# Optimization experiments

Measured on AMD Instinct MI355X. Metric: run time of the kernel, lower is better.

## Reference

```python
import jax, jax.numpy as jnp
import numpy as np

K = 7      # number of neighbor volumes (init k)
PS = 7     # patch size (unfold.ps / wpsum.ps)
WS = 13    # search window side -> O = WS*WS candidates per query
WR = WS // 2
EPS = 1e-6


def setup_inputs() -> dict:
    key = jax.random.key(0)
    k1, k2, k3, k4 = jax.random.split(key, 4)
    C, E, H, W = 64, 32, 128, 128
    return {
        "x": jax.random.normal(k1, (C, H, W), jnp.float32),
        "xe": jax.random.normal(k2, (E, H, W), jnp.float32),
        "ye": jax.random.normal(k3, (E, H, W), jnp.float32),
        "log_temp": 0.1 * jax.random.normal(k4, (1, H, W), jnp.float32),
    }


def _box_sum(img, ps):
    # img: [B, H, W] -> centered ps x ps box sum with zero padding, same shape
    kern = jnp.ones((1, 1, ps, ps), img.dtype)
    return jax.lax.conv_general_dilated(img[:, None], kern, (1, 1), "SAME")[:, 0]


def _forward(x, xe, ye, log_temp):
    C, H, W_ = x.shape
    E = xe.shape[0]
    offs = np.stack(np.meshgrid(np.arange(WS), np.arange(WS), indexing="ij"), -1).reshape(-1, 2)
    O = offs.shape[0]
    dis = jnp.asarray(offs[:, 0]); djs = jnp.asarray(offs[:, 1])

    xe_pad = jnp.pad(xe, ((0, 0), (WR, WR), (WR, WR)))
    x_pad = jnp.pad(x, ((0, 0), (WR, WR), (WR, WR)))

    # ---- search: per-candidate patch SSD between query/database embeddings ----
    def per_off_dist(di, dj):
        xs = jax.lax.dynamic_slice(xe_pad, (0, di, dj), (E, H, W_))
        return jnp.sum((ye - xs) ** 2, axis=0)  # [H, W] pixel-wise sq dist

    diff2 = jax.vmap(per_off_dist)(dis, djs)        # [O, H, W]
    dists = -_box_sum(diff2, PS)                    # patch SSD, negated

    # ---- temperature: avgpool of log_temp over the ps x ps patch (avgpool=True) ----
    lt = _box_sum(log_temp, PS) / float(PS * PS)    # [1, H, W]
    temp = jnp.exp(lt)                              # temp_bias=1 -> log bias 0

    # ---- NeuralNearestNeighbors: k rounds of temp-softmax with exclusion ----
    logits = dists / temp                           # [O, H, W]
    Ws = []
    for _ in range(K):  # small structural loop over k neighbor volumes
        w = jax.nn.softmax(logits, axis=0)
        Ws.append(w)
        logits = logits + jnp.log(jnp.clip(1.0 - w, EPS))
    Wk = jnp.stack(Ws, 0)                           # [K, O, H, W]

    # ---- wpsum + fold fused: for stride-1 centered patches the patch offset
    # cancels, so out[k,c,y] = sum_o boxsum_ps(W[k,o])[y] * x[c, y + off(o)] ----
    Wsum = _box_sum(Wk.reshape(K * O, H, W_), PS).reshape(K, O, H, W_)
    Wsum_o = jnp.moveaxis(Wsum, 1, 0)               # [O, K, H, W]

    def body(out, inp):
        di, dj, wso = inp
        xs = jax.lax.dynamic_slice(x_pad, (0, di, dj), (C, H, W_))
        return out + wso[:, None] * xs[None], None  # [K, C, H, W]

    out0 = jnp.zeros((K, C, H, W_), x.dtype)
    out, _ = jax.lax.scan(body, out0, (dis, djs, Wsum_o))
    return out.reshape(K * C, H, W_)


def reference(x, xe, ye, log_temp):
    return _forward(x, xe, ye, log_temp)
```

## Files before the change

### kernel.cpp

```cpp
#include <hip/hip_runtime.h>
#include <hip/hip_bf16.h>
#include <hip/hip_fp16.h>

#define HW 16384

using u16 = unsigned short;
using u32 = unsigned int;
typedef __attribute__((ext_vector_type(2))) float f32x2;

__device__ __forceinline__ u16 f2h(float f) {
    __half h = __float2half(f);
    return __builtin_bit_cast(u16, h);
}
__device__ __forceinline__ void dot2acc(float& acc, u32 a, u32 b) {
    asm("v_dot2_f32_f16 %0, %1, %2, %0" : "+v"(acc) : "v"(a), "v"(b));
}
#define SELLO 0x05040100u
#define SELHI 0x07060302u

__global__ __launch_bounds__(256) void k_prep(
        const float* __restrict__ x, const float* __restrict__ xe,
        const float* __restrict__ ye,
        u16* __restrict__ xh, float* __restrict__ xeT,
        float* __restrict__ yeT, float* __restrict__ nx, float* __restrict__ ny) {
    int y = blockIdx.x * 256 + threadIdx.x;

#pragma unroll
    for (int c = 0; c < 64; c++)
        xh[c * HW + y] = f2h(x[c * HW + y]);

    float sx = 0.f, sy = 0.f;
#pragma unroll
    for (int e0 = 0; e0 < 32; e0 += 4) {
        float4 v = make_float4(xe[(e0 + 0) * HW + y], xe[(e0 + 1) * HW + y],
                               xe[(e0 + 2) * HW + y], xe[(e0 + 3) * HW + y]);
        *reinterpret_cast<float4*>(xeT + y * 32 + e0) = v;
        sx += v.x * v.x + v.y * v.y + v.z * v.z + v.w * v.w;
        float4 u = make_float4(ye[(e0 + 0) * HW + y], ye[(e0 + 1) * HW + y],
                               ye[(e0 + 2) * HW + y], ye[(e0 + 3) * HW + y]);
        *reinterpret_cast<float4*>(yeT + y * 32 + e0) = u;
        sy += u.x * u.x + u.y * u.y + u.z * u.z + u.w * u.w;
    }
    nx[y] = sx;
    ny[y] = sy;
}

__global__ __launch_bounds__(256) void k_norms(
        const float* __restrict__ ny, const float* __restrict__ lt,
        float2* __restrict__ st) {
    int y = blockIdx.x * 256 + threadIdx.x;
    int py = y >> 7, px = y & 127;
    float s = 0.f, t = 0.f;
    for (int dy = -3; dy <= 3; dy++)
        for (int dx = -3; dx <= 3; dx++) {
            int yy = py + dy, xx = px + dx;
            if ((unsigned)yy < 128u && (unsigned)xx < 128u) {
                int p = yy * 128 + xx;
                s += ny[p];
                t += lt[p];
            }
        }
    float tinv = __expf(-t * (1.0f / 49.0f));
    st[y] = make_float2(tinv, tinv * s);
}

__global__ __launch_bounds__(1024) void k_logits(
        const float* __restrict__ xeT, const float* __restrict__ yeT,
        const float* __restrict__ nxg, const float2* __restrict__ st,
        float* __restrict__ logits) {
#pragma clang fp contract(fast)
    __shared__ __align__(16) char arena[123904];
    float* s_xe = (float*)arena;
    float* s_nx = (float*)(arena + 95744);
    float* s_d2 = (float*)(arena + 98736);
    float* s_hs = (float*)arena;

    int di = blockIdx.x;
    int tile = blockIdx.y;
    int h0 = (tile >> 3) * 16, w0 = (tile & 7) * 16;
    int gr0 = h0 + di - 9, gc0 = w0 - 9;
    int tid = threadIdx.x;

    for (int idx = tid; idx < 748 * 8; idx += 1024) {
        int cell = idx >> 3, q = idx & 7;
        int r = cell / 34, c = cell - r * 34;
        int gy = gr0 + r, gx = gc0 + c;
        float4 v = make_float4(0.f, 0.f, 0.f, 0.f);
        if ((unsigned)gy < 128u && (unsigned)gx < 128u)
            v = *reinterpret_cast<const float4*>(xeT + (size_t)(gy * 128 + gx) * 32 + q * 4);
        *reinterpret_cast<float4*>(s_xe + cell * 32 + ((q ^ (cell & 7)) << 2)) = v;
    }
    for (int idx = tid; idx < 748; idx += 1024) {
        int r = idx / 34, c = idx - r * 34;
        int gy = gr0 + r, gx = gc0 + c;
        float v = 0.f;
        if ((unsigned)gy < 128u && (unsigned)gx < 128u) v = nxg[gy * 128 + gx];
        s_nx[idx] = v;
    }
    __syncthreads();

    if (tid < 484) {
        int zr = tid / 22, zc = tid - zr * 22;
        int gy = h0 - 3 + zr, gx = w0 - 3 + zc;
        bool zin = ((unsigned)gy < 128u) && ((unsigned)gx < 128u);
        f32x2 yv[16];
#pragma unroll
        for (int j = 0; j < 16; j++) yv[j] = (f32x2){0.f, 0.f};
        if (zin) {
            const float* yp = yeT + (size_t)(gy * 128 + gx) * 32;
#pragma unroll
            for (int j = 0; j < 8; j++) {
                float4 t = *reinterpret_cast<const float4*>(yp + j * 4);
                yv[2 * j] = (f32x2){t.x, t.y};
                yv[2 * j + 1] = (f32x2){t.z, t.w};
            }
        }
        int cell0 = zr * 34 + zc;
#pragma unroll
        for (int dj = 0; dj < 13; dj++) {
            int cell = cell0 + dj;
            const float* bp = s_xe + cell * 32;
            int sw = cell & 7;
            f32x2 a0 = {0.f, 0.f}, a1 = {0.f, 0.f};
#pragma unroll
            for (int q = 0; q < 8; q++) {
                float4 xv = *reinterpret_cast<const float4*>(bp + ((q ^ sw) << 2));
                a0 += ((f32x2){xv.x, xv.y}) * yv[2 * q];
                a1 += ((f32x2){xv.z, xv.w}) * yv[2 * q + 1];
            }
            float cr = a0.x + a0.y + a1.x + a1.y;
            float d2v = fmaf(-2.f, cr, s_nx[cell]);
            s_d2[dj * 484 + tid] = zin ? d2v : 0.f;
        }
    }
    __syncthreads();

    for (int idx = tid; idx < 4576; idx += 1024) {
        int dj = idx / 352, rem = idx - dj * 352;
        int r = rem >> 4, c = rem & 15;
        const float* p = s_d2 + dj * 484 + r * 22 + c;
        float s = p[0] + p[1] + p[2] + p[3] + p[4] + p[5] + p[6];
        s_hs[(dj * 22 + r) * 16 + c] = s;
    }
    __syncthreads();

    for (int idx = tid; idx < 3328; idx += 1024) {
        int dj = idx >> 8, rem = idx & 255;
        int i = rem >> 4, jj = rem & 15;
        const float* p = s_hs + (dj * 22 + i) * 16 + jj;
        float s = p[0] + p[16] + p[32] + p[48] + p[64] + p[80] + p[96];
        int y = (h0 + i) * 128 + (w0 + jj);
        float2 ab = st[y];
        logits[(di * 13 + dj) * HW + y] = -fmaf(ab.x, s, ab.y);
    }
}

__global__ __launch_bounds__(256) void k_softmax(
        const float* __restrict__ logits, u16* __restrict__ Wkt) {
    __shared__ float s_lg[169 * 34];
    int tid = threadIdx.x;
    int y0 = blockIdx.x * 32;
    for (int idx = tid; idx < 169 * 32; idx += 256) {
        int o = idx >> 5, p = idx & 31;
        s_lg[o * 34 + p] = logits[o * HW + y0 + p];
    }
    __syncthreads();
    int pix = tid >> 3, t = tid & 7;
    int y = y0 + pix;
    float l[22];
#pragma unroll
    for (int j = 0; j < 22; j++) {
        int o = t + 8 * j;
        l[j] = (o < 169) ? s_lg[o * 34 + pix] : -3e38f;
    }
    u32 wp0[22], wp1[22], wp2[22], wp3[22];
#pragma unroll
    for (int j = 0; j < 22; j++) { wp0[j] = 0u; wp1[j] = 0u; wp2[j] = 0u; wp3[j] = 0u; }

    float e[22];
#pragma unroll
    for (int k = 0; k < 7; k++) {
        float m = -3e38f;
#pragma unroll
        for (int j = 0; j < 22; j++) m = fmaxf(m, l[j]);
        m = fmaxf(m, __shfl_xor(m, 1));
        m = fmaxf(m, __shfl_xor(m, 2));
        m = fmaxf(m, __shfl_xor(m, 4));
        float s = 0.f;
#pragma unroll
        for (int j = 0; j < 22; j++) { e[j] = __expf(l[j] - m); s += e[j]; }
        s += __shfl_xor(s, 1);
        s += __shfl_xor(s, 2);
        s += __shfl_xor(s, 4);
        float rs = 1.0f / s;
#pragma unroll
        for (int j = 0; j < 22; j++) {
            float w = e[j] * rs;
            u32 h = (u32)f2h(w);
            if (k == 0) wp0[j] |= h;
            else if (k == 1) wp0[j] |= h << 16;
            else if (k == 2) wp1[j] |= h;
            else if (k == 3) wp1[j] |= h << 16;
            else if (k == 4) wp2[j] |= h;
            else if (k == 5) wp2[j] |= h << 16;
            else wp3[j] |= h;
            if (k < 6) l[j] += __logf(fmaxf(1.0f - w, 1e-6f));
        }
    }
#pragma unroll
    for (int j = 0; j < 22; j++) {
        int o = t + 8 * j;
        if (o < 169)
            *reinterpret_cast<uint4*>(Wkt + (o * HW + y) * 8) =
                make_uint4(wp0[j], wp1[j], wp2[j], wp3[j]);
    }
}

__global__ __launch_bounds__(256) void k_wsum(
        const u16* __restrict__ Wkt, u32* __restrict__ WsP) {
    __shared__ u16 s_w[38 * 39 * 8];
    __shared__ u16 s_v[32 * 38 * 8];
    int o2 = blockIdx.x;
    int di = o2 / 7, djp = o2 - di * 7;
    int oA = di * 13 + 2 * djp;
    bool hasB = (djp < 6);
    int tile = blockIdx.y;
    int h0 = (tile >> 2) * 32, w0 = (tile & 3) * 32;
    int tid = threadIdx.x;

    auto stage = [&](int o) {
        const u16* src = Wkt + (size_t)o * (HW * 8);
        for (int idx = tid; idx < 38 * 38; idx += 256) {
            int r = idx / 38, c = idx - r * 38;
            int gy = h0 - 3 + r, gx = w0 - 3 + c;
            uint4 v = make_uint4(0u, 0u, 0u, 0u);
            if ((unsigned)gy < 128u && (unsigned)gx < 128u)
                v = *reinterpret_cast<const uint4*>(src + (gy * 128 + gx) * 8);
            *reinterpret_cast<uint4*>(s_w + (r * 39 + c) * 8) = v;
        }
    };
    auto vert = [&]() {
        for (int u = tid; u < 1216; u += 256) {
            int r = u / 38, c = u - r * 38;
            __half2 s0 = __builtin_bit_cast(__half2, 0u);
            __half2 s1 = s0, s2 = s0, s3 = s0;
#pragma unroll
            for (int d = 0; d < 7; d++) {
                uint4 q = *reinterpret_cast<const uint4*>(s_w + ((r + d) * 39 + c) * 8);
                s0 = __hadd2(s0, __builtin_bit_cast(__half2, q.x));
                s1 = __hadd2(s1, __builtin_bit_cast(__half2, q.y));
                s2 = __hadd2(s2, __builtin_bit_cast(__half2, q.z));
                s3 = __hadd2(s3, __builtin_bit_cast(__half2, q.w));
            }
            *reinterpret_cast<uint4*>(s_v + (r * 38 + c) * 8) = make_uint4(
                __builtin_bit_cast(u32, s0), __builtin_bit_cast(u32, s1),
                __builtin_bit_cast(u32, s2), __builtin_bit_cast(u32, s3));
        }
    };
    auto horiz = [&](uint4 (&rr)[4]) {
#pragma unroll
        for (int i = 0; i < 4; i++) {
            int u = tid + i * 256;
            int r = u >> 5, cx = u & 31;
            __half2 s0 = __builtin_bit_cast(__half2, 0u);
            __half2 s1 = s0, s2 = s0, s3 = s0;
#pragma unroll
            for (int d = 0; d < 7; d++) {
                uint4 q = *reinterpret_cast<const uint4*>(s_v + (r * 38 + cx + d) * 8);
                s0 = __hadd2(s0, __builtin_bit_cast(__half2, q.x));
                s1 = __hadd2(s1, __builtin_bit_cast(__half2, q.y));
                s2 = __hadd2(s2, __builtin_bit_cast(__half2, q.z));
                s3 = __hadd2(s3, __builtin_bit_cast(__half2, q.w));
            }
            rr[i] = make_uint4(
                __builtin_bit_cast(u32, s0), __builtin_bit_cast(u32, s1),
                __builtin_bit_cast(u32, s2), __builtin_bit_cast(u32, s3));
        }
    };

    uint4 rA[4], rB[4];
#pragma unroll
    for (int i = 0; i < 4; i++) rB[i] = make_uint4(0u, 0u, 0u, 0u);

    stage(oA);
    __syncthreads();
    vert();
    __syncthreads();
    horiz(rA);
    if (hasB) {
        __syncthreads();
        stage(oA + 1);
        __syncthreads();
        vert();
        __syncthreads();
        horiz(rB);
    }

#pragma unroll
    for (int i = 0; i < 4; i++) {
        int u = tid + i * 256;
        int r = u >> 5, cx = u & 31;
        int y = (h0 + r) * 128 + (w0 + cx);
        u32* dst = WsP + ((size_t)o2 * HW + y) * 8;
        uint4 lo = make_uint4(
            __builtin_amdgcn_perm(rB[i].x, rA[i].x, SELLO),
            __builtin_amdgcn_perm(rB[i].x, rA[i].x, SELHI),
            __builtin_amdgcn_perm(rB[i].y, rA[i].y, SELLO),
            __builtin_amdgcn_perm(rB[i].y, rA[i].y, SELHI));
        uint4 hi = make_uint4(
            __builtin_amdgcn_perm(rB[i].z, rA[i].z, SELLO),
            __builtin_amdgcn_perm(rB[i].z, rA[i].z, SELHI),
            __builtin_amdgcn_perm(rB[i].w, rA[i].w, SELLO),
            0u);
        *reinterpret_cast<uint4*>(dst) = lo;
        *reinterpret_cast<uint4*>(dst + 4) = hi;
    }
}

__global__ __launch_bounds__(512, 2) void k_agg(
        const u16* __restrict__ xh, const u32* __restrict__ WsP,
        float* __restrict__ out) {
    __shared__ u16 s_x[64 * 16 * 32];
    int tb = blockIdx.x;
    int h0 = (tb >> 3) * 4, w0 = (tb & 7) * 16;
    int tid = threadIdx.x;

#pragma unroll
    for (int i = 0; i < 8; i++) {
        int it = tid + i * 512;
        int ch = it >> 6;
        int r = (it >> 2) & 15;
        int c0 = (it & 3) * 8;
        int gy = h0 - 6 + r, gx0 = w0 - 6 + c0;
        uint4 v = make_uint4(0u, 0u, 0u, 0u);
        if ((unsigned)gy < 128u) {
            const u16* src = xh + (size_t)ch * HW + gy * 128;
            if (gx0 >= 0 && gx0 <= 120) {
                v = *reinterpret_cast<const uint4*>(src + gx0);
            } else {
                auto pk = [&](int gx) -> u32 {
                    u32 lo = ((unsigned)gx < 128u) ? (u32)src[gx] : 0u;
                    u32 hi = ((unsigned)(gx + 1) < 128u) ? (u32)src[gx + 1] : 0u;
                    return lo | (hi << 16);
                };
                v = make_uint4(pk(gx0), pk(gx0 + 2), pk(gx0 + 4), pk(gx0 + 6));
            }
        }
        *reinterpret_cast<uint4*>(s_x + (ch * 16 + r) * 32 + c0) = v;
    }
    __syncthreads();

    int cc = tid >> 6, pix = tid & 63;
    int pr = pix >> 4, pc = pix & 15;
    int y = (h0 + pr) * 128 + (w0 + pc);
    const u32* wsrc = WsP + (size_t)y * 8;
    const u32* s_x32 = reinterpret_cast<const u32*>(s_x);
    u32 sh = (u32)(pc & 1) * 16;
    int base0 = cc * 8 * 256 + (pc >> 1);

    float acc[7][8];
#pragma unroll
    for (int k = 0; k < 7; k++)
#pragma unroll
        for (int q = 0; q < 8; q++) acc[k][q] = 0.f;

    auto loadW = [&](int di, uint4 (&A)[7], uint4 (&B)[7]) {
        const u32* wdi = wsrc + (size_t)(di * 7) * (HW * 8);
#pragma unroll
        for (int djp = 0; djp < 7; djp++) {
            const u32* wp = wdi + (size_t)djp * (HW * 8);
            A[djp] = *reinterpret_cast<const uint4*>(wp);
            B[djp] = *reinterpret_cast<const uint4*>(wp + 4);
        }
    };
    auto compute = [&](int di, const uint4 (&A)[7], const uint4 (&B)[7]) {
        int rowoff = (pr + di) * 16;
#pragma unroll
        for (int q = 0; q < 8; q++) {
            const u32* p = s_x32 + base0 + q * 256 + rowoff;
            u32 f0 = p[0], f1 = p[1], f2 = p[2], f3 = p[3];
            u32 f4 = p[4], f5 = p[5], f6 = p[6], f7 = p[7];
            u32 x2;
            x2 = __builtin_amdgcn_alignbit(f1, f0, sh);
            dot2acc(acc[0][q], A[0].x, x2); dot2acc(acc[1][q], A[0].y, x2);
            dot2acc(acc[2][q], A[0].z, x2); dot2acc(acc[3][q], A[0].w, x2);
            dot2acc(acc[4][q], B[0].x, x2); dot2acc(acc[5][q], B[0].y, x2);
            dot2acc(acc[6][q], B[0].z, x2);
            x2 = __builtin_amdgcn_alignbit(f2, f1, sh);
            dot2acc(acc[0][q], A[1].x, x2); dot2acc(acc[1][q], A[1].y, x2);
            dot2acc(acc[2][q], A[1].z, x2); dot2acc(acc[3][q], A[1].w, x2);
            dot2acc(acc[4][q], B[1].x, x2); dot2acc(acc[5][q], B[1].y, x2);
            dot2acc(acc[6][q], B[1].z, x2);
            x2 = __builtin_amdgcn_alignbit(f3, f2, sh);
            dot2acc(acc[0][q], A[2].x, x2); dot2acc(acc[1][q], A[2].y, x2);
            dot2acc(acc[2][q], A[2].z, x2); dot2acc(acc[3][q], A[2].w, x2);
            dot2acc(acc[4][q], B[2].x, x2); dot2acc(acc[5][q], B[2].y, x2);
            dot2acc(acc[6][q], B[2].z, x2);
            x2 = __builtin_amdgcn_alignbit(f4, f3, sh);
            dot2acc(acc[0][q], A[3].x, x2); dot2acc(acc[1][q], A[3].y, x2);
            dot2acc(acc[2][q], A[3].z, x2); dot2acc(acc[3][q], A[3].w, x2);
            dot2acc(acc[4][q], B[3].x, x2); dot2acc(acc[5][q], B[3].y, x2);
            dot2acc(acc[6][q], B[3].z, x2);
            x2 = __builtin_amdgcn_alignbit(f5, f4, sh);
            dot2acc(acc[0][q], A[4].x, x2); dot2acc(acc[1][q], A[4].y, x2);
            dot2acc(acc[2][q], A[4].z, x2); dot2acc(acc[3][q], A[4].w, x2);
            dot2acc(acc[4][q], B[4].x, x2); dot2acc(acc[5][q], B[4].y, x2);
            dot2acc(acc[6][q], B[4].z, x2);
            x2 = __builtin_amdgcn_alignbit(f6, f5, sh);
            dot2acc(acc[0][q], A[5].x, x2); dot2acc(acc[1][q], A[5].y, x2);
            dot2acc(acc[2][q], A[5].z, x2); dot2acc(acc[3][q], A[5].w, x2);
            dot2acc(acc[4][q], B[5].x, x2); dot2acc(acc[5][q], B[5].y, x2);
            dot2acc(acc[6][q], B[5].z, x2);
            x2 = __builtin_amdgcn_alignbit(f7, f6, sh);
            dot2acc(acc[0][q], A[6].x, x2); dot2acc(acc[1][q], A[6].y, x2);
            dot2acc(acc[2][q], A[6].z, x2); dot2acc(acc[3][q], A[6].w, x2);
            dot2acc(acc[4][q], B[6].x, x2); dot2acc(acc[5][q], B[6].y, x2);
            dot2acc(acc[6][q], B[6].z, x2);
        }
    };

    uint4 WA[7], WB[7], WC[7], WD[7];
    loadW(0, WA, WB);
#pragma unroll 1
    for (int di = 0; di < 12; di += 2) {
        loadW(di + 1, WC, WD);
        compute(di, WA, WB);
        loadW(di + 2, WA, WB);
        compute(di + 1, WC, WD);
    }
    compute(12, WA, WB);

#pragma unroll
    for (int k = 0; k < 7; k++)
#pragma unroll
        for (int q = 0; q < 8; q++)
            out[(k * 64 + cc * 8 + q) * HW + y] = acc[k][q];
}

extern "C" void kernel_launch(void* const* d_in, const int* in_sizes, int n_in,
                              void* d_out, int out_size, void* d_ws, size_t ws_size,
                              hipStream_t stream) {
    (void)in_sizes; (void)n_in; (void)out_size; (void)ws_size;
    const float* x  = (const float*)d_in[0];
    const float* xe = (const float*)d_in[1];
    const float* ye = (const float*)d_in[2];
    const float* lt = (const float*)d_in[3];
    float* out = (float*)d_out;
    char* ws = (char*)d_ws;

    u16*   xh     = (u16*)(ws + 0);
    float* xeT    = (float*)(ws + 2097152u);
    float* yeT    = (float*)(ws + 4194304u);
    u16*   Wkt    = (u16*)(ws + 6291456u);
    float* logits = (float*)(ws + 50593792u);
    u32*   WsP    = (u32*)(ws + 50593792u);
    float*  nx = (float*)(ws + 6291456u);
    float*  ny = (float*)(ws + 6291456u + 65536u);
    float2* st = (float2*)(ws + 6291456u + 131072u);

    k_prep<<<64, 256, 0, stream>>>(x, xe, ye, xh, xeT, yeT, nx, ny);
    k_norms<<<64, 256, 0, stream>>>(ny, lt, st);
    k_logits<<<dim3(13, 64), 1024, 0, stream>>>(xeT, yeT, nx, st, logits);
    k_softmax<<<512, 256, 0, stream>>>(logits, Wkt);
    k_wsum<<<dim3(91, 16), 256, 0, stream>>>(Wkt, WsP);
    k_agg<<<256, 512, 0, stream>>>(xh, WsP, out);
}
```

Baseline: 155.2 us.

## Split logits embedding dimension into two halves across blocks, combine in softmax

```diff
diff --git a/kernel.cpp b/kernel.cpp
--- a/kernel.cpp
+++ b/kernel.cpp
@@ -22,26 +22,28 @@
         const float* __restrict__ x, const float* __restrict__ xe,
         const float* __restrict__ ye,
         u16* __restrict__ xh, float* __restrict__ xeT,
-        float* __restrict__ yeT, float* __restrict__ nx, float* __restrict__ ny) {
+        float* __restrict__ yeT, float* __restrict__ nx2, float* __restrict__ ny) {
     int y = blockIdx.x * 256 + threadIdx.x;
 
 #pragma unroll
     for (int c = 0; c < 64; c++)
         xh[c * HW + y] = f2h(x[c * HW + y]);
 
-    float sx = 0.f, sy = 0.f;
+    float sx0 = 0.f, sx1 = 0.f, sy = 0.f;
 #pragma unroll
     for (int e0 = 0; e0 < 32; e0 += 4) {
         float4 v = make_float4(xe[(e0 + 0) * HW + y], xe[(e0 + 1) * HW + y],
                                xe[(e0 + 2) * HW + y], xe[(e0 + 3) * HW + y]);
         *reinterpret_cast<float4*>(xeT + y * 32 + e0) = v;
-        sx += v.x * v.x + v.y * v.y + v.z * v.z + v.w * v.w;
+        float s = v.x * v.x + v.y * v.y + v.z * v.z + v.w * v.w;
+        if (e0 < 16) sx0 += s; else sx1 += s;
         float4 u = make_float4(ye[(e0 + 0) * HW + y], ye[(e0 + 1) * HW + y],
                                ye[(e0 + 2) * HW + y], ye[(e0 + 3) * HW + y]);
         *reinterpret_cast<float4*>(yeT + y * 32 + e0) = u;
         sy += u.x * u.x + u.y * u.y + u.z * u.z + u.w * u.w;
     }
-    nx[y] = sx;
+    nx2[y] = sx0;
+    nx2[HW + y] = sx1;
     ny[y] = sy;
 }
 
@@ -66,35 +68,37 @@
 
 __global__ __launch_bounds__(1024) void k_logits(
         const float* __restrict__ xeT, const float* __restrict__ yeT,
-        const float* __restrict__ nxg, const float2* __restrict__ st,
-        float* __restrict__ logits) {
+        const float* __restrict__ nx2, float* __restrict__ lg) {
 #pragma clang fp contract(fast)
-    __shared__ __align__(16) char arena[123904];
+    __shared__ __align__(16) char arena[76032];
     float* s_xe = (float*)arena;
-    float* s_nx = (float*)(arena + 95744);
-    float* s_d2 = (float*)(arena + 98736);
+    float* s_nx = (float*)(arena + 47872);
+    float* s_d2 = (float*)(arena + 50864);
     float* s_hs = (float*)arena;
 
     int di = blockIdx.x;
     int tile = blockIdx.y;
+    int h = blockIdx.z;
     int h0 = (tile >> 3) * 16, w0 = (tile & 7) * 16;
     int gr0 = h0 + di - 9, gc0 = w0 - 9;
     int tid = threadIdx.x;
 
-    for (int idx = tid; idx < 748 * 8; idx += 1024) {
-        int cell = idx >> 3, q = idx & 7;
+    for (int idx = tid; idx < 748 * 4; idx += 1024) {
+        int cell = idx >> 2, q = idx & 3;
         int r = cell / 34, c = cell - r * 34;
         int gy = gr0 + r, gx = gc0 + c;
         float4 v = make_float4(0.f, 0.f, 0.f, 0.f);
         if ((unsigned)gy < 128u && (unsigned)gx < 128u)
-            v = *reinterpret_cast<const float4*>(xeT + (size_t)(gy * 128 + gx) * 32 + q * 4);
-        *reinterpret_cast<float4*>(s_xe + cell * 32 + ((q ^ (cell & 7)) << 2)) = v;
+            v = *reinterpret_cast<const float4*>(
+                    xeT + (size_t)(gy * 128 + gx) * 32 + h * 16 + q * 4);
+        *reinterpret_cast<float4*>(s_xe + cell * 16 + ((q ^ (cell & 3)) << 2)) = v;
     }
     for (int idx = tid; idx < 748; idx += 1024) {
         int r = idx / 34, c = idx - r * 34;
         int gy = gr0 + r, gx = gc0 + c;
         float v = 0.f;
-        if ((unsigned)gy < 128u && (unsigned)gx < 128u) v = nxg[gy * 128 + gx];
+        if ((unsigned)gy < 128u && (unsigned)gx < 128u)
+            v = nx2[h * HW + gy * 128 + gx];
         s_nx[idx] = v;
     }
     __syncthreads();
@@ -103,13 +107,13 @@
         int zr = tid / 22, zc = tid - zr * 22;
         int gy = h0 - 3 + zr, gx = w0 - 3 + zc;
         bool zin = ((unsigned)gy < 128u) && ((unsigned)gx < 128u);
-        f32x2 yv[16];
-#pragma unroll
-        for (int j = 0; j < 16; j++) yv[j] = (f32x2){0.f, 0.f};
+        f32x2 yv[8];
+#pragma unroll
+        for (int j = 0; j < 8; j++) yv[j] = (f32x2){0.f, 0.f};
         if (zin) {
-            const float* yp = yeT + (size_t)(gy * 128 + gx) * 32;
-#pragma unroll
-            for (int j = 0; j < 8; j++) {
+            const float* yp = yeT + (size_t)(gy * 128 + gx) * 32 + h * 16;
+#pragma unroll
+            for (int j = 0; j < 4; j++) {
                 float4 t = *reinterpret_cast<const float4*>(yp + j * 4);
                 yv[2 * j] = (f32x2){t.x, t.y};
                 yv[2 * j + 1] = (f32x2){t.z, t.w};
@@ -119,11 +123,11 @@
 #pragma unroll
         for (int dj = 0; dj < 13; dj++) {
             int cell = cell0 + dj;
-            const float* bp = s_xe + cell * 32;
-            int sw = cell & 7;
+            const float* bp = s_xe + cell * 16;
+            int sw = cell & 3;
             f32x2 a0 = {0.f, 0.f}, a1 = {0.f, 0.f};
 #pragma unroll
-            for (int q = 0; q < 8; q++) {
+            for (int q = 0; q < 4; q++) {
                 float4 xv = *reinterpret_cast<const float4*>(bp + ((q ^ sw) << 2));
                 a0 += ((f32x2){xv.x, xv.y}) * yv[2 * q];
                 a1 += ((f32x2){xv.z, xv.w}) * yv[2 * q + 1];
@@ -150,28 +154,30 @@
         const float* p = s_hs + (dj * 22 + i) * 16 + jj;
         float s = p[0] + p[16] + p[32] + p[48] + p[64] + p[80] + p[96];
         int y = (h0 + i) * 128 + (w0 + jj);
-        float2 ab = st[y];
-        logits[(di * 13 + dj) * HW + y] = -fmaf(ab.x, s, ab.y);
+        lg[((size_t)h * 169 + di * 13 + dj) * HW + y] = s;
     }
 }
 
 __global__ __launch_bounds__(256) void k_softmax(
-        const float* __restrict__ logits, u16* __restrict__ Wkt) {
+        const float* __restrict__ lg, const float2* __restrict__ st,
+        u16* __restrict__ Wkt) {
     __shared__ float s_lg[169 * 34];
     int tid = threadIdx.x;
     int y0 = blockIdx.x * 32;
     for (int idx = tid; idx < 169 * 32; idx += 256) {
         int o = idx >> 5, p = idx & 31;
-        s_lg[o * 34 + p] = logits[o * HW + y0 + p];
+        s_lg[o * 34 + p] = lg[(size_t)o * HW + y0 + p]
+                         + lg[(size_t)(169 + o) * HW + y0 + p];
     }
     __syncthreads();
     int pix = tid >> 3, t = tid & 7;
     int y = y0 + pix;
+    float2 ab = st[y];
     float l[22];
 #pragma unroll
     for (int j = 0; j < 22; j++) {
         int o = t + 8 * j;
-        l[j] = (o < 169) ? s_lg[o * 34 + pix] : -3e38f;
+        l[j] = (o < 169) ? -fmaf(ab.x, s_lg[o * 34 + pix], ab.y) : -3e38f;
     }
     u32 wp0[22], wp1[22], wp2[22], wp3[22];
 #pragma unroll
@@ -196,14 +202,14 @@
 #pragma unroll
         for (int j = 0; j < 22; j++) {
             float w = e[j] * rs;
-            u32 h = (u32)f2h(w);
-            if (k == 0) wp0[j] |= h;
-            else if (k == 1) wp0[j] |= h << 16;
-            else if (k == 2) wp1[j] |= h;
-            else if (k == 3) wp1[j] |= h << 16;
-            else if (k == 4) wp2[j] |= h;
-            else if (k == 5) wp2[j] |= h << 16;
-            else wp3[j] |= h;
+            u32 hh = (u32)f2h(w);
+            if (k == 0) wp0[j] |= hh;
+            else if (k == 1) wp0[j] |= hh << 16;
+            else if (k == 2) wp1[j] |= hh;
+            else if (k == 3) wp1[j] |= hh << 16;
+            else if (k == 4) wp2[j] |= hh;
+            else if (k == 5) wp2[j] |= hh << 16;
+            else wp3[j] |= hh;
             if (k < 6) l[j] += __logf(fmaxf(1.0f - w, 1e-6f));
         }
     }
@@ -211,7 +217,7 @@
     for (int j = 0; j < 22; j++) {
         int o = t + 8 * j;
         if (o < 169)
-            *reinterpret_cast<uint4*>(Wkt + (o * HW + y) * 8) =
+            *reinterpret_cast<uint4*>(Wkt + ((size_t)o * HW + y) * 8) =
                 make_uint4(wp0[j], wp1[j], wp2[j], wp3[j]);
     }
 }
@@ -448,20 +454,20 @@
     float* out = (float*)d_out;
     char* ws = (char*)d_ws;
 
-    u16*   xh     = (u16*)(ws + 0);
-    float* xeT    = (float*)(ws + 2097152u);
-    float* yeT    = (float*)(ws + 4194304u);
-    u16*   Wkt    = (u16*)(ws + 6291456u);
-    float* logits = (float*)(ws + 50593792u);
-    u32*   WsP    = (u32*)(ws + 50593792u);
-    float*  nx = (float*)(ws + 6291456u);
-    float*  ny = (float*)(ws + 6291456u + 65536u);
-    float2* st = (float2*)(ws + 6291456u + 131072u);
-
-    k_prep<<<64, 256, 0, stream>>>(x, xe, ye, xh, xeT, yeT, nx, ny);
+    u16*    xh  = (u16*)(ws + 0);
+    float*  xeT = (float*)(ws + 2097152u);
+    float*  yeT = (float*)(ws + 4194304u);
+    u16*    Wkt = (u16*)(ws + 6291456u);
+    float*  lg  = (float*)(ws + 50593792u);
+    u32*    WsP = (u32*)(ws + 72744960u);
+    float*  nx2 = (float*)(ws + 120455168u);
+    float*  ny  = (float*)(ws + 120586240u);
+    float2* st  = (float2*)(ws + 120651776u);
+
+    k_prep<<<64, 256, 0, stream>>>(x, xe, ye, xh, xeT, yeT, nx2, ny);
     k_norms<<<64, 256, 0, stream>>>(ny, lt, st);
-    k_logits<<<dim3(13, 64), 1024, 0, stream>>>(xeT, yeT, nx, st, logits);
-    k_softmax<<<512, 256, 0, stream>>>(logits, Wkt);
+    k_logits<<<dim3(13, 64, 2), 1024, 0, stream>>>(xeT, yeT, nx2, lg);
+    k_softmax<<<512, 256, 0, stream>>>(lg, st, Wkt);
     k_wsum<<<dim3(91, 16), 256, 0, stream>>>(Wkt, WsP);
     k_agg<<<256, 512, 0, stream>>>(xh, WsP, out);
 }
```

Result: faster. 140.5 us (-9.5%).
